# Performance work log

Measured on AMD Instinct MI355X. Metric: run time of the kernel, lower is better.

The kernel has to match this reference:

```python
import jax, jax.numpy as jnp
import numpy as np

K_TOP = 2          # hardcoded k in MyAttentionFunction
S = 32             # hardcoded spatial size (interpolate to 32x32)
N = S * S          # 1024 patches (patch_size=1, stride=1 unfold)
NEG = jnp.float32(-1e30)  # stand-in for excluding columns from top-k


def setup_inputs() -> dict:
    key = jax.random.key(0)
    k1, k2, k3 = jax.random.split(key, 3)
    C = 4096
    generated = jax.random.normal(k1, (1, C, S, S), dtype=jnp.float32)
    known = jax.random.normal(k2, (1, C, S, S), dtype=jnp.float32)
    mask = jax.random.randint(k3, (1, 1, S, S), 0, 2).astype(jnp.float32)
    return {"generated": generated, "known": known, "mask": mask}


def _forward(generated, known, mask):
    C = generated.shape[1]
    # F.interpolate(mask, (32,32)) nearest, then flatten -> flag in {0,1}, shape (N,)
    flag = jax.image.resize(mask, (1, 1, S, S), method="nearest").reshape(N)
    # MyUnfold(x, 1, 1) == [1, N, C]; drop batch dim of 1.
    P = generated.reshape(C, N).T   # (N, C) patches of `generated`
    Kp = known.reshape(C, N).T      # (N, C) patches of `known`

    norm_p = jnp.sum(P * P, axis=-1)   # (N,)
    norm_k = jnp.sum(Kp * Kp, axis=-1)
    # Full cosine matrices; original restricts rows to flag==1 and columns to
    # flag==0 (cosine0) / flag==1 (cosine1) by extraction; we mask columns with
    # a very negative value so top-k returns the same values with GLOBAL indices
    # (which is exactly what the original reconstructs via nonzero()[indexes]).
    cos0 = (P @ Kp.T) / jnp.sqrt(norm_p[:, None] * norm_k[None, :])  # (N, N)
    cos1 = (P @ P.T) / jnp.sqrt(norm_p[:, None] * norm_p[None, :])
    cos0 = jnp.where(flag[None, :] == 0, cos0, NEG)
    cos1 = jnp.where(flag[None, :] == 1, cos1, NEG)

    w0, i0 = jax.lax.top_k(cos0, K_TOP)  # (N, k) values / global indices
    w1, i1 = jax.lax.top_k(cos1, K_TOP)

    m = flag                      # 1.0 on masked rows
    nm = jnp.sum(m)               # number of masked patches
    # weight means taken only over masked rows, then softmax (original uses
    # .item() + numpy softmax, i.e. detached constants).
    means = jnp.stack(
        [jnp.sum(w0[:, i] * m) / nm for i in range(K_TOP)]
        + [jnp.sum(w1[:, i] * m) / nm for i in range(K_TOP)]
    )
    weights = jax.lax.stop_gradient(jax.nn.softmax(means))  # (2k,)

    # The original builds dense 1024x1024 indicator matrices and bmm's them;
    # each indicator row for a masked patch is one-hot at its retrieved source,
    # so the bmm is just a gather into masked rows. The advanced-indexing quirk
    # ind[mask_idx, src_idx] (nonzero() pairs include a leading 0 column) also
    # unconditionally sets ind[0,0]=1; we reproduce that (set semantics: no
    # double count if row 0 already maps to column 0).
    rtn = jnp.zeros((N, C), dtype=generated.dtype)
    for i in range(2 * K_TOP):
        src = Kp if i < K_TOP else P
        cols = (i0 if i < K_TOP else i1)[:, i % K_TOP]  # (N,) global indices
        out_i = jnp.where(m[:, None] == 1, src[cols], 0.0)  # masked rows only
        dup = 1.0 - ((m[0] == 1) & (cols[0] == 0)).astype(src.dtype)
        out_i = out_i.at[0].add(src[0] * dup)  # spurious ind[0,0]=1 artifact
        rtn = rtn + weights[i] * out_i

    rtn = rtn.reshape(1, S, S, C).transpose(0, 3, 1, 2)  # (1, C, 32, 32)
    return jnp.concatenate([generated, known, rtn], axis=1)


def reference(generated, known, mask):
    return _forward(generated, known, mask)
```

## Files before the change

kernel.cpp:

```cpp
#include <hip/hip_runtime.h>
#include <hip/hip_bf16.h>
#include <math.h>

#define N_TOT 1024
#define C_DIM 4096
#define T_MARGIN 3e-4f

typedef __attribute__((ext_vector_type(8))) _Float16 half8;
typedef __attribute__((ext_vector_type(8))) unsigned short ushort8;
typedef __attribute__((ext_vector_type(8))) char schar8;
typedef __attribute__((ext_vector_type(4))) float floatx4;

__device__ inline unsigned short f2h(float v) {
    _Float16 h = (_Float16)v;
    return __builtin_bit_cast(unsigned short, h);
}
__device__ inline float h2f(unsigned short u) {
    return (float)__builtin_bit_cast(_Float16, u);
}
__device__ inline char lo_enc(float v, unsigned short h) {
    int e = (h >> 10) & 31;
    float lo = v - h2f(h);
    float q = rintf(lo * 240.0f * __uint_as_float((unsigned)(152 - e) << 23));
    q = fmaxf(-127.0f, fminf(127.0f, q));
    return (char)(int)q;
}
__device__ inline float lo_dec(char q, unsigned short h) {
    int e = (h >> 10) & 31;
    return (float)q * __uint_as_float((unsigned)(e + 102) << 23) * (1.0f / 240.0f);
}

__global__ __launch_bounds__(256) void flagscan(const float* __restrict__ flag,
                                                int* __restrict__ colidx,
                                                int* __restrict__ n0p) {
    __shared__ int cz[256];
    __shared__ int co[256];
    const int t = threadIdx.x;
    float4 fv = *(const float4*)&flag[4 * t];
    int f[4] = {fv.x == 0.0f, fv.y == 0.0f, fv.z == 0.0f, fv.w == 0.0f};
    int nz = f[0] + f[1] + f[2] + f[3];
    cz[t] = nz; co[t] = 4 - nz;
    __syncthreads();
    for (int off = 1; off < 256; off <<= 1) {
        int vz = (t >= off) ? cz[t - off] : 0;
        int vo = (t >= off) ? co[t - off] : 0;
        __syncthreads();
        cz[t] += vz; co[t] += vo;
        __syncthreads();
    }
    const int n0 = cz[255];
    int zs = cz[t] - nz;
    int os = n0 + co[t] - (4 - nz);
    #pragma unroll
    for (int e = 0; e < 4; e++) {
        int j = 4 * t + e;
        if (f[e]) colidx[zs++] = j;
        else      colidx[os++] = j;
    }
    if (t == 0) *n0p = n0;
}

__global__ __launch_bounds__(256) void split_norms(const float* __restrict__ G,
                                                   const float* __restrict__ Kn,
                                                   unsigned short* __restrict__ Phi,
                                                   char* __restrict__ Plo,
                                                   unsigned short* __restrict__ Khi,
                                                   char* __restrict__ Klo,
                                                   float* __restrict__ normP,
                                                   float* __restrict__ normK) {
    const int z = blockIdx.z;
    const float* X = z ? Kn : G;
    unsigned short* Xhi = z ? Khi : Phi;
    char* Xlo = z ? Klo : Plo;
    float* normX = z ? normK : normP;

    __shared__ float tile[64 * 65];
    __shared__ float np[256];
    const int t  = threadIdx.x;
    const int c0 = blockIdx.x * 64;
    const int n0 = blockIdx.y * 64;

    float s2 = 0.0f;
    #pragma unroll
    for (int s = 0; s < 16; s++) {
        int c_loc = s * 4 + (t >> 6);
        int n_loc = t & 63;
        float v = X[(c0 + c_loc) * N_TOT + n0 + n_loc];
        tile[c_loc * 65 + n_loc] = v;
        s2 = fmaf(v, v, s2);
    }
    np[t] = s2;
    __syncthreads();

    if (t < 64) {
        float tot = np[t] + np[t + 64] + np[t + 128] + np[t + 192];
        atomicAdd(&normX[n0 + t], tot);
    }

    #pragma unroll
    for (int s = 0; s < 4; s++) {
        int n_loc = s * 16 + (t >> 4);
        int c4    = (t & 15) * 4;
        unsigned short h[4]; char l[4];
        #pragma unroll
        for (int e = 0; e < 4; e++) {
            float v = tile[(c4 + e) * 65 + n_loc];
            h[e] = f2h(v);
            l[e] = lo_enc(v, h[e]);
        }
        size_t base = (size_t)(n0 + n_loc) * C_DIM + c0 + c4;
        *(ushort4*)&Xhi[base] = make_ushort4(h[0], h[1], h[2], h[3]);
        *(char4*)&Xlo[base]   = make_char4(l[0], l[1], l[2], l[3]);
    }
}

__global__ __launch_bounds__(256, 4) void gemm_coarse(const unsigned short* __restrict__ Phi,
                                                      const unsigned short* __restrict__ Khi,
                                                      const int* __restrict__ colidx,
                                                      const int* __restrict__ n0p,
                                                      float* __restrict__ dotSel) {
    __shared__ unsigned short sA[64 * 64];
    __shared__ unsigned short sB[128 * 64];

    const int t    = threadIdx.x;
    const int wave = t >> 6, lane = t & 63;
    const int wm   = wave >> 1, wn = wave & 1;
    const int quad = lane >> 4, lrow = lane & 15;
    const int ib = blockIdx.x * 64, jb = blockIdx.y * 128;
    const int k_beg = blockIdx.z * 512;
    const int n0 = *n0p;

    const int srow = t >> 3;
    const int g    = (t & 7) ^ (srow & 7);

    const unsigned short* gA[2];
    gA[0] = Phi + (size_t)(ib + srow) * C_DIM + g * 8;
    gA[1] = gA[0] + (size_t)32 * C_DIM;
    const unsigned short* gB[4];
    #pragma unroll
    for (int q = 0; q < 4; q++) {
        int s = jb + q * 32 + srow;
        int row = colidx[s];
        const unsigned short* src = (s < n0) ? Khi : Phi;
        gB[q] = src + (size_t)row * C_DIM + g * 8;
    }

    floatx4 acc[2][4] = {};

    for (int k0 = k_beg; k0 < k_beg + 512; k0 += 64) {
        #pragma unroll
        for (int q = 0; q < 2; q++)
            __builtin_amdgcn_global_load_lds(
                (const __attribute__((address_space(1))) void*)(gA[q] + k0),
                (__attribute__((address_space(3))) void*)((char*)sA + q * 4096 + t * 16), 16, 0, 0);
        #pragma unroll
        for (int q = 0; q < 4; q++)
            __builtin_amdgcn_global_load_lds(
                (const __attribute__((address_space(1))) void*)(gB[q] + k0),
                (__attribute__((address_space(3))) void*)((char*)sB + q * 4096 + t * 16), 16, 0, 0);
        __syncthreads();

        #pragma unroll
        for (int kk = 0; kk < 2; kk++) {
            const int gk = kk * 4 + quad;
            half8 a[2], b[4];
            #pragma unroll
            for (int ti = 0; ti < 2; ti++) {
                int m = wm * 32 + ti * 16 + lrow;
                a[ti] = *(const half8*)&sA[m * 64 + ((gk ^ (m & 7)) << 3)];
            }
            #pragma unroll
            for (int tj = 0; tj < 4; tj++) {
                int n = wn * 64 + tj * 16 + lrow;
                b[tj] = *(const half8*)&sB[n * 64 + ((gk ^ (n & 7)) << 3)];
            }
            #pragma unroll
            for (int ti = 0; ti < 2; ti++)
                #pragma unroll
                for (int tj = 0; tj < 4; tj++)
                    acc[ti][tj] = __builtin_amdgcn_mfma_f32_16x16x32_f16(a[ti], b[tj], acc[ti][tj], 0, 0, 0);
        }
        __syncthreads();
    }

    #pragma unroll
    for (int tj = 0; tj < 4; tj++) {
        int j = jb + wn * 64 + tj * 16 + lrow;
        #pragma unroll
        for (int ti = 0; ti < 2; ti++) {
            #pragma unroll
            for (int reg = 0; reg < 4; reg++) {
                int i = ib + wm * 32 + ti * 16 + quad * 4 + reg;
                atomicAdd(&dotSel[(size_t)i * N_TOT + j], acc[ti][tj][reg]);
            }
        }
    }
}

__global__ __launch_bounds__(256) void topk_refine(const float* __restrict__ dotSel,
                                                   const unsigned short* __restrict__ Phi,
                                                   const char* __restrict__ Plo,
                                                   const unsigned short* __restrict__ Khi,
                                                   const char* __restrict__ Klo,
                                                   const float* __restrict__ normP,
                                                   const float* __restrict__ normK,
                                                   const int* __restrict__ colidx,
                                                   const int* __restrict__ n0p,
                                                   float* __restrict__ w01,
                                                   int* __restrict__ i01) {
    __shared__ float sAf[C_DIM];
    __shared__ float s_bv[4];
    __shared__ int   s_bj[4];
    __shared__ float s_rcv[8];

    const int row = blockIdx.x;
    const int z   = blockIdx.y;
    const int t   = threadIdx.x;
    const int wave = t >> 6, lane = t & 63;
    const int n0 = *n0p;
    const float nr = normP[row];

    float4 dv = *(const float4*)&dotSel[(size_t)row * N_TOT + 4 * t];
    float cv[4];
    #pragma unroll
    for (int e = 0; e < 4; e++) {
        int s = 4 * t + e;
        bool inz = z ? (s >= n0) : (s < n0);
        if (inz) {
            int gj = colidx[s];
            float nb = (s < n0) ? normK[gj] : normP[gj];
            cv[e] = dv[e] * rsqrtf(nr * nb);
        } else cv[e] = -INFINITY;
    }

    int   cand[8];
    float cval[8];
    #pragma unroll
    for (int it = 0; it < 8; it++) {
        float bv = cv[0]; int bj = 4 * t;
        #pragma unroll
        for (int e = 1; e < 4; e++) {
            int j = 4 * t + e;
            if (cv[e] > bv || (cv[e] == bv && j < bj)) { bv = cv[e]; bj = j; }
        }
        #pragma unroll
        for (int off = 32; off > 0; off >>= 1) {
            float ov = __shfl_xor(bv, off);
            int   oj = __shfl_xor(bj, off);
            if (ov > bv || (ov == bv && oj < bj)) { bv = ov; bj = oj; }
        }
        if (lane == 0) { s_bv[wave] = bv; s_bj[wave] = bj; }
        __syncthreads();
        float wv = s_bv[0]; int wj = s_bj[0];
        #pragma unroll
        for (int w = 1; w < 4; w++)
            if (s_bv[w] > wv || (s_bv[w] == wv && s_bj[w] < wj)) { wv = s_bv[w]; wj = s_bj[w]; }
        cand[it] = wj; cval[it] = wv;
        #pragma unroll
        for (int e = 0; e < 4; e++)
            if (wj == 4 * t + e) cv[e] = -INFINITY;
        __syncthreads();
    }

    const bool trust = (cval[0] - cval[1] > T_MARGIN) && (cval[1] - cval[2] > T_MARGIN);
    if (trust) {
        if (t == 0) {
            int base = (z * N_TOT + row) * 2;
            w01[base]     = cval[0];
            w01[base + 1] = cval[1];
            i01[base]     = colidx[cand[0]];
            i01[base + 1] = colidx[cand[1]];
        }
        return;
    }

    {
        const unsigned short* Ah = Phi + (size_t)row * C_DIM;
        const char*           Al = Plo + (size_t)row * C_DIM;
        #pragma unroll
        for (int s = 0; s < 2; s++) {
            int c = t * 16 + s * 8;
            ushort8 hb = *(const ushort8*)&Ah[c];
            schar8  lb = *(const schar8*)&Al[c];
            #pragma unroll
            for (int e = 0; e < 8; e++) sAf[c + e] = h2f(hb[e]) + lo_dec(lb[e], hb[e]);
        }
    }
    __syncthreads();

    const int grp = t >> 5, l32 = t & 31;
    const int cs  = cand[grp];
    const int gj  = colidx[cs];
    const unsigned short* bh_row = ((cs < n0) ? Khi : Phi) + (size_t)gj * C_DIM;
    const char*           bl_row = ((cs < n0) ? Klo : Plo) + (size_t)gj * C_DIM;
    float acc = 0.0f;
    for (int it = 0; it < 16; it++) {
        int c = it * 256 + l32 * 8;
        ushort8 hb = *(const ushort8*)&bh_row[c];
        schar8  lb = *(const schar8*)&bl_row[c];
        #pragma unroll
        for (int e = 0; e < 8; e++)
            acc = fmaf(sAf[c + e], h2f(hb[e]) + lo_dec(lb[e], hb[e]), acc);
    }
    #pragma unroll
    for (int off = 16; off > 0; off >>= 1) acc += __shfl_xor(acc, off);
    if (l32 == 0) s_rcv[grp] = acc;
    __syncthreads();

    if (t == 0) {
        float v1 = -INFINITY, v2 = -INFINITY;
        int   j1 = 0x7FFFFFFF, j2 = 0x7FFFFFFF;
        #pragma unroll
        for (int q = 0; q < 8; q++) {
            if (!(cval[q] > -1e29f)) continue;
            int s = cand[q];
            int gjx = colidx[s];
            float nb = (s < n0) ? normK[gjx] : normP[gjx];
            float cvx = s_rcv[q] * rsqrtf(nr * nb);
            int j = gjx;
            if (cvx > v1 || (cvx == v1 && j < j1)) {
                v2 = v1; j2 = j1; v1 = cvx; j1 = j;
            } else if (cvx > v2 || (cvx == v2 && j < j2)) {
                v2 = cvx; j2 = j;
            }
        }
        int base = (z * N_TOT + row) * 2;
        w01[base]     = v1;
        w01[base + 1] = v2;
        i01[base]     = j1;
        i01[base + 1] = j2;
    }
}

__global__ __launch_bounds__(256) void output_kernel(const float* __restrict__ G,
                                                     const float* __restrict__ Kn,
                                                     const float* __restrict__ flag,
                                                     const float* __restrict__ w01,
                                                     const int* __restrict__ i01,
                                                     float* __restrict__ out) {
    __shared__ float red[5][4];
    __shared__ float wts[4];
    const int c  = blockIdx.x;
    const int t  = threadIdx.x;
    const int n4 = t * 4;

    float4 fv = *(const float4*)&flag[n4];
    const float fa[4] = {fv.x, fv.y, fv.z, fv.w};

    float pm[5] = {};
    #pragma unroll
    for (int e = 0; e < 4; e++) {
        int n = n4 + e;
        float m = fa[e];
        pm[0] += m;
        pm[1] += m * w01[n * 2 + 0];
        pm[2] += m * w01[n * 2 + 1];
        pm[3] += m * w01[2 * N_TOT + n * 2 + 0];
        pm[4] += m * w01[2 * N_TOT + n * 2 + 1];
    }
    #pragma unroll
    for (int i = 0; i < 5; i++)
        #pragma unroll
        for (int off = 32; off > 0; off >>= 1)
            pm[i] += __shfl_xor(pm[i], off);
    const int wave = t >> 6, lane = t & 63;
    if (lane == 0) {
        #pragma unroll
        for (int i = 0; i < 5; i++) red[i][wave] = pm[i];
    }
    __syncthreads();
    if (t == 0) {
        float tot[5];
        #pragma unroll
        for (int i = 0; i < 5; i++)
            tot[i] = red[i][0] + red[i][1] + red[i][2] + red[i][3];
        float inv = 1.0f / tot[0];
        float mv[4] = {tot[1] * inv, tot[2] * inv, tot[3] * inv, tot[4] * inv};
        float mx = fmaxf(fmaxf(mv[0], mv[1]), fmaxf(mv[2], mv[3]));
        float e[4], s = 0.0f;
        #pragma unroll
        for (int q = 0; q < 4; q++) { e[q] = expf(mv[q] - mx); s += e[q]; }
        #pragma unroll
        for (int q = 0; q < 4; q++) wts[q] = e[q] / s;
    }
    __syncthreads();
    const float w0 = wts[0], w1 = wts[1], w2 = wts[2], w3 = wts[3];

    float4 gv = *(const float4*)&G[c * N_TOT + n4];
    float4 kv = *(const float4*)&Kn[c * N_TOT + n4];
    *(float4*)&out[c * N_TOT + n4] = gv;
    *(float4*)&out[C_DIM * N_TOT + c * N_TOT + n4] = kv;

    float val[4];
    #pragma unroll
    for (int e = 0; e < 4; e++) {
        int n = n4 + e;
        float v = 0.0f;
        if (fa[e] == 1.0f) {
            int c00 = i01[n * 2 + 0];
            int c01 = i01[n * 2 + 1];
            int c10 = i01[2 * N_TOT + n * 2 + 0];
            int c11 = i01[2 * N_TOT + n * 2 + 1];
            v = w0 * Kn[c * N_TOT + c00] + w1 * Kn[c * N_TOT + c01]
              + w2 * G[c * N_TOT + c10]  + w3 * G[c * N_TOT + c11];
        }
        if (n == 0) {
            bool m0 = (flag[0] == 1.0f);
            int c00 = i01[0], c01 = i01[1];
            int c10 = i01[2 * N_TOT], c11 = i01[2 * N_TOT + 1];
            float kn0 = Kn[c * N_TOT];
            float g0  = G[c * N_TOT];
            if (!(m0 && c00 == 0)) v += w0 * kn0;
            if (!(m0 && c01 == 0)) v += w1 * kn0;
            if (!(m0 && c10 == 0)) v += w2 * g0;
            if (!(m0 && c11 == 0)) v += w3 * g0;
        }
        val[e] = v;
    }
    *(float4*)&out[2 * C_DIM * N_TOT + c * N_TOT + n4] =
        make_float4(val[0], val[1], val[2], val[3]);
}

extern "C" void kernel_launch(void* const* d_in, const int* in_sizes, int n_in,
                              void* d_out, int out_size, void* d_ws, size_t ws_size,
                              hipStream_t stream) {
    const float* G    = (const float*)d_in[0];
    const float* Kn   = (const float*)d_in[1];
    const float* flag = (const float*)d_in[2];
    float* out = (float*)d_out;

    char* p = (char*)d_ws;
    unsigned short* Phi = (unsigned short*)p;  p += (size_t)N_TOT * C_DIM * 2;
    unsigned short* Khi = (unsigned short*)p;  p += (size_t)N_TOT * C_DIM * 2;
    char* Plo = p;                             p += (size_t)N_TOT * C_DIM;
    char* Klo = p;                             p += (size_t)N_TOT * C_DIM;
    float* dotSel = (float*)p;                 p += (size_t)N_TOT * N_TOT * 4;
    float* normP  = (float*)p;                 p += N_TOT * 4;
    float* normK  = (float*)p;                 p += N_TOT * 4;
    float* w01    = (float*)p;                 p += 4 * N_TOT * 4;
    int*   i01    = (int*)p;                   p += 4 * N_TOT * 4;
    int*   colidx = (int*)p;                   p += N_TOT * 4;
    int*   n0p    = (int*)p;

    const size_t zero_bytes = ((size_t)N_TOT * N_TOT + 2 * N_TOT) * sizeof(float);
    hipMemsetAsync(dotSel, 0, zero_bytes, stream);

    flagscan<<<1, 256, 0, stream>>>(flag, colidx, n0p);
    split_norms<<<dim3(64, 16, 2), 256, 0, stream>>>(G, Kn, Phi, Plo, Khi, Klo, normP, normK);
    gemm_coarse<<<dim3(16, 8, 8), 256, 0, stream>>>(Phi, Khi, colidx, n0p, dotSel);
    topk_refine<<<dim3(1024, 2), 256, 0, stream>>>(dotSel, Phi, Plo, Khi, Klo,
                                                   normP, normK, colidx, n0p, w01, i01);
    output_kernel<<<4096, 256, 0, stream>>>(G, Kn, flag, w01, i01, out);
}
```

Measured before the change: 186.0 us.

## Replace split-K atomics with partial buffers, fuse flagscan, merge top-k passes

The GEMM's split-K slices now write plain stores into eight separate partial buffers instead of atomically adding into one zeroed matrix. The top-k kernel sums those partials once per row and handles both column groups in a single block. This removes the 4MB memset, the atomic traffic and the duplicate dot-row reads. The flag scan is folded into the first block of split_norms to save a launch, at the cost of 32MB of extra partial-buffer writes and reads.

```diff
diff --git a/kernel.cpp b/kernel.cpp
--- a/kernel.cpp
+++ b/kernel.cpp
@@ -30,44 +30,17 @@
     return (float)q * __uint_as_float((unsigned)(e + 102) << 23) * (1.0f / 240.0f);
 }
 
-__global__ __launch_bounds__(256) void flagscan(const float* __restrict__ flag,
-                                                int* __restrict__ colidx,
-                                                int* __restrict__ n0p) {
-    __shared__ int cz[256];
-    __shared__ int co[256];
-    const int t = threadIdx.x;
-    float4 fv = *(const float4*)&flag[4 * t];
-    int f[4] = {fv.x == 0.0f, fv.y == 0.0f, fv.z == 0.0f, fv.w == 0.0f};
-    int nz = f[0] + f[1] + f[2] + f[3];
-    cz[t] = nz; co[t] = 4 - nz;
-    __syncthreads();
-    for (int off = 1; off < 256; off <<= 1) {
-        int vz = (t >= off) ? cz[t - off] : 0;
-        int vo = (t >= off) ? co[t - off] : 0;
-        __syncthreads();
-        cz[t] += vz; co[t] += vo;
-        __syncthreads();
-    }
-    const int n0 = cz[255];
-    int zs = cz[t] - nz;
-    int os = n0 + co[t] - (4 - nz);
-    #pragma unroll
-    for (int e = 0; e < 4; e++) {
-        int j = 4 * t + e;
-        if (f[e]) colidx[zs++] = j;
-        else      colidx[os++] = j;
-    }
-    if (t == 0) *n0p = n0;
-}
-
 __global__ __launch_bounds__(256) void split_norms(const float* __restrict__ G,
                                                    const float* __restrict__ Kn,
+                                                   const float* __restrict__ flag,
                                                    unsigned short* __restrict__ Phi,
                                                    char* __restrict__ Plo,
                                                    unsigned short* __restrict__ Khi,
                                                    char* __restrict__ Klo,
                                                    float* __restrict__ normP,
-                                                   float* __restrict__ normK) {
+                                                   float* __restrict__ normK,
+                                                   int* __restrict__ colidx,
+                                                   int* __restrict__ n0p) {
     const int z = blockIdx.z;
     const float* X = z ? Kn : G;
     unsigned short* Xhi = z ? Khi : Phi;
@@ -112,13 +85,40 @@
         *(ushort4*)&Xhi[base] = make_ushort4(h[0], h[1], h[2], h[3]);
         *(char4*)&Xlo[base]   = make_char4(l[0], l[1], l[2], l[3]);
     }
+
+    if (blockIdx.x == 0 && blockIdx.y == 0 && blockIdx.z == 0) {
+        __shared__ int cz[256];
+        __shared__ int co[256];
+        float4 fv = *(const float4*)&flag[4 * t];
+        int f[4] = {fv.x == 0.0f, fv.y == 0.0f, fv.z == 0.0f, fv.w == 0.0f};
+        int nz = f[0] + f[1] + f[2] + f[3];
+        cz[t] = nz; co[t] = 4 - nz;
+        __syncthreads();
+        for (int off = 1; off < 256; off <<= 1) {
+            int vz = (t >= off) ? cz[t - off] : 0;
+            int vo = (t >= off) ? co[t - off] : 0;
+            __syncthreads();
+            cz[t] += vz; co[t] += vo;
+            __syncthreads();
+        }
+        const int fn0 = cz[255];
+        int zs = cz[t] - nz;
+        int os = fn0 + co[t] - (4 - nz);
+        #pragma unroll
+        for (int e = 0; e < 4; e++) {
+            int j = 4 * t + e;
+            if (f[e]) colidx[zs++] = j;
+            else      colidx[os++] = j;
+        }
+        if (t == 0) *n0p = fn0;
+    }
 }
 
 __global__ __launch_bounds__(256, 4) void gemm_coarse(const unsigned short* __restrict__ Phi,
                                                       const unsigned short* __restrict__ Khi,
                                                       const int* __restrict__ colidx,
                                                       const int* __restrict__ n0p,
-                                                      float* __restrict__ dotSel) {
+                                                      float* __restrict__ dotPart) {
     __shared__ unsigned short sA[64 * 64];
     __shared__ unsigned short sB[128 * 64];
 
@@ -127,7 +127,8 @@
     const int wm   = wave >> 1, wn = wave & 1;
     const int quad = lane >> 4, lrow = lane & 15;
     const int ib = blockIdx.x * 64, jb = blockIdx.y * 128;
-    const int k_beg = blockIdx.z * 512;
+    const int bz = blockIdx.z;
+    const int k_beg = bz * 512;
     const int n0 = *n0p;
 
     const int srow = t >> 3;
@@ -183,6 +184,7 @@
         __syncthreads();
     }
 
+    float* outp = dotPart + ((size_t)bz << 20);
     #pragma unroll
     for (int tj = 0; tj < 4; tj++) {
         int j = jb + wn * 64 + tj * 16 + lrow;
@@ -191,13 +193,13 @@
             #pragma unroll
             for (int reg = 0; reg < 4; reg++) {
                 int i = ib + wm * 32 + ti * 16 + quad * 4 + reg;
-                atomicAdd(&dotSel[(size_t)i * N_TOT + j], acc[ti][tj][reg]);
-            }
-        }
-    }
-}
-
-__global__ __launch_bounds__(256) void topk_refine(const float* __restrict__ dotSel,
+                outp[i * N_TOT + j] = acc[ti][tj][reg];
+            }
+        }
+    }
+}
+
+__global__ __launch_bounds__(256) void topk_refine(const float* __restrict__ dotPart,
                                                    const unsigned short* __restrict__ Phi,
                                                    const char* __restrict__ Plo,
                                                    const unsigned short* __restrict__ Khi,
@@ -214,65 +216,80 @@
     __shared__ float s_rcv[8];
 
     const int row = blockIdx.x;
-    const int z   = blockIdx.y;
     const int t   = threadIdx.x;
     const int wave = t >> 6, lane = t & 63;
     const int n0 = *n0p;
     const float nr = normP[row];
 
-    float4 dv = *(const float4*)&dotSel[(size_t)row * N_TOT + 4 * t];
+    float4 dv = make_float4(0.f, 0.f, 0.f, 0.f);
+    #pragma unroll
+    for (int z = 0; z < 8; z++) {
+        float4 p = *(const float4*)&dotPart[((size_t)z << 20) + (size_t)row * N_TOT + 4 * t];
+        dv.x += p.x; dv.y += p.y; dv.z += p.z; dv.w += p.w;
+    }
+
     float cv[4];
     #pragma unroll
     for (int e = 0; e < 4; e++) {
         int s = 4 * t + e;
-        bool inz = z ? (s >= n0) : (s < n0);
-        if (inz) {
-            int gj = colidx[s];
-            float nb = (s < n0) ? normK[gj] : normP[gj];
-            cv[e] = dv[e] * rsqrtf(nr * nb);
-        } else cv[e] = -INFINITY;
-    }
-
-    int   cand[8];
-    float cval[8];
-    #pragma unroll
-    for (int it = 0; it < 8; it++) {
-        float bv = cv[0]; int bj = 4 * t;
-        #pragma unroll
-        for (int e = 1; e < 4; e++) {
-            int j = 4 * t + e;
-            if (cv[e] > bv || (cv[e] == bv && j < bj)) { bv = cv[e]; bj = j; }
-        }
-        #pragma unroll
-        for (int off = 32; off > 0; off >>= 1) {
-            float ov = __shfl_xor(bv, off);
-            int   oj = __shfl_xor(bj, off);
-            if (ov > bv || (ov == bv && oj < bj)) { bv = ov; bj = oj; }
-        }
-        if (lane == 0) { s_bv[wave] = bv; s_bj[wave] = bj; }
-        __syncthreads();
-        float wv = s_bv[0]; int wj = s_bj[0];
-        #pragma unroll
-        for (int w = 1; w < 4; w++)
-            if (s_bv[w] > wv || (s_bv[w] == wv && s_bj[w] < wj)) { wv = s_bv[w]; wj = s_bj[w]; }
-        cand[it] = wj; cval[it] = wv;
-        #pragma unroll
-        for (int e = 0; e < 4; e++)
-            if (wj == 4 * t + e) cv[e] = -INFINITY;
-        __syncthreads();
-    }
-
-    const bool trust = (cval[0] - cval[1] > T_MARGIN) && (cval[1] - cval[2] > T_MARGIN);
-    if (trust) {
-        if (t == 0) {
-            int base = (z * N_TOT + row) * 2;
-            w01[base]     = cval[0];
-            w01[base + 1] = cval[1];
-            i01[base]     = colidx[cand[0]];
-            i01[base + 1] = colidx[cand[1]];
-        }
-        return;
-    }
+        int gj = colidx[s];
+        float nb = (s < n0) ? normK[gj] : normP[gj];
+        float d  = (e == 0) ? dv.x : (e == 1) ? dv.y : (e == 2) ? dv.z : dv.w;
+        cv[e] = d * rsqrtf(nr * nb);
+    }
+
+    int   candZ[2][8];
+    float cvalZ[2][8];
+    bool  need[2];
+
+    #pragma unroll
+    for (int zz = 0; zz < 2; zz++) {
+        float mv[4];
+        #pragma unroll
+        for (int e = 0; e < 4; e++) {
+            int s = 4 * t + e;
+            bool inz = zz ? (s >= n0) : (s < n0);
+            mv[e] = inz ? cv[e] : -INFINITY;
+        }
+        #pragma unroll
+        for (int it = 0; it < 8; it++) {
+            float bv = mv[0]; int bj = 4 * t;
+            #pragma unroll
+            for (int e = 1; e < 4; e++) {
+                int j = 4 * t + e;
+                if (mv[e] > bv || (mv[e] == bv && j < bj)) { bv = mv[e]; bj = j; }
+            }
+            #pragma unroll
+            for (int off = 32; off > 0; off >>= 1) {
+                float ov = __shfl_xor(bv, off);
+                int   oj = __shfl_xor(bj, off);
+                if (ov > bv || (ov == bv && oj < bj)) { bv = ov; bj = oj; }
+            }
+            if (lane == 0) { s_bv[wave] = bv; s_bj[wave] = bj; }
+            __syncthreads();
+            float wv = s_bv[0]; int wj = s_bj[0];
+            #pragma unroll
+            for (int w = 1; w < 4; w++)
+                if (s_bv[w] > wv || (s_bv[w] == wv && s_bj[w] < wj)) { wv = s_bv[w]; wj = s_bj[w]; }
+            candZ[zz][it] = wj; cvalZ[zz][it] = wv;
+            #pragma unroll
+            for (int e = 0; e < 4; e++)
+                if (wj == 4 * t + e) mv[e] = -INFINITY;
+            __syncthreads();
+        }
+        const bool trust = (cvalZ[zz][0] - cvalZ[zz][1] > T_MARGIN) &&
+                           (cvalZ[zz][1] - cvalZ[zz][2] > T_MARGIN);
+        need[zz] = !trust;
+        if (trust && t == 0) {
+            int base = (zz * N_TOT + row) * 2;
+            w01[base]     = cvalZ[zz][0];
+            w01[base + 1] = cvalZ[zz][1];
+            i01[base]     = colidx[candZ[zz][0]];
+            i01[base + 1] = colidx[candZ[zz][1]];
+        }
+    }
+
+    if (!need[0] && !need[1]) return;
 
     {
         const unsigned short* Ah = Phi + (size_t)row * C_DIM;
@@ -288,47 +305,52 @@
     }
     __syncthreads();
 
-    const int grp = t >> 5, l32 = t & 31;
-    const int cs  = cand[grp];
-    const int gj  = colidx[cs];
-    const unsigned short* bh_row = ((cs < n0) ? Khi : Phi) + (size_t)gj * C_DIM;
-    const char*           bl_row = ((cs < n0) ? Klo : Plo) + (size_t)gj * C_DIM;
-    float acc = 0.0f;
-    for (int it = 0; it < 16; it++) {
-        int c = it * 256 + l32 * 8;
-        ushort8 hb = *(const ushort8*)&bh_row[c];
-        schar8  lb = *(const schar8*)&bl_row[c];
-        #pragma unroll
-        for (int e = 0; e < 8; e++)
-            acc = fmaf(sAf[c + e], h2f(hb[e]) + lo_dec(lb[e], hb[e]), acc);
-    }
-    #pragma unroll
-    for (int off = 16; off > 0; off >>= 1) acc += __shfl_xor(acc, off);
-    if (l32 == 0) s_rcv[grp] = acc;
-    __syncthreads();
-
-    if (t == 0) {
-        float v1 = -INFINITY, v2 = -INFINITY;
-        int   j1 = 0x7FFFFFFF, j2 = 0x7FFFFFFF;
-        #pragma unroll
-        for (int q = 0; q < 8; q++) {
-            if (!(cval[q] > -1e29f)) continue;
-            int s = cand[q];
-            int gjx = colidx[s];
-            float nb = (s < n0) ? normK[gjx] : normP[gjx];
-            float cvx = s_rcv[q] * rsqrtf(nr * nb);
-            int j = gjx;
-            if (cvx > v1 || (cvx == v1 && j < j1)) {
-                v2 = v1; j2 = j1; v1 = cvx; j1 = j;
-            } else if (cvx > v2 || (cvx == v2 && j < j2)) {
-                v2 = cvx; j2 = j;
-            }
-        }
-        int base = (z * N_TOT + row) * 2;
-        w01[base]     = v1;
-        w01[base + 1] = v2;
-        i01[base]     = j1;
-        i01[base + 1] = j2;
+    #pragma unroll
+    for (int zz = 0; zz < 2; zz++) {
+        if (!need[zz]) continue;
+        const int grp = t >> 5, l32 = t & 31;
+        const int cs  = candZ[zz][grp];
+        const int gj  = colidx[cs];
+        const unsigned short* bh_row = ((cs < n0) ? Khi : Phi) + (size_t)gj * C_DIM;
+        const char*           bl_row = ((cs < n0) ? Klo : Plo) + (size_t)gj * C_DIM;
+        float acc = 0.0f;
+        for (int it = 0; it < 16; it++) {
+            int c = it * 256 + l32 * 8;
+            ushort8 hb = *(const ushort8*)&bh_row[c];
+            schar8  lb = *(const schar8*)&bl_row[c];
+            #pragma unroll
+            for (int e = 0; e < 8; e++)
+                acc = fmaf(sAf[c + e], h2f(hb[e]) + lo_dec(lb[e], hb[e]), acc);
+        }
+        #pragma unroll
+        for (int off = 16; off > 0; off >>= 1) acc += __shfl_xor(acc, off);
+        if (l32 == 0) s_rcv[grp] = acc;
+        __syncthreads();
+
+        if (t == 0) {
+            float v1 = -INFINITY, v2 = -INFINITY;
+            int   j1 = 0x7FFFFFFF, j2 = 0x7FFFFFFF;
+            #pragma unroll
+            for (int q = 0; q < 8; q++) {
+                if (!(cvalZ[zz][q] > -1e29f)) continue;
+                int s = candZ[zz][q];
+                int gjx = colidx[s];
+                float nb = (s < n0) ? normK[gjx] : normP[gjx];
+                float cvx = s_rcv[q] * rsqrtf(nr * nb);
+                int j = gjx;
+                if (cvx > v1 || (cvx == v1 && j < j1)) {
+                    v2 = v1; j2 = j1; v1 = cvx; j1 = j;
+                } else if (cvx > v2 || (cvx == v2 && j < j2)) {
+                    v2 = cvx; j2 = j;
+                }
+            }
+            int base = (zz * N_TOT + row) * 2;
+            w01[base]     = v1;
+            w01[base + 1] = v2;
+            i01[base]     = j1;
+            i01[base + 1] = j2;
+        }
+        __syncthreads();
     }
 }
 
@@ -434,7 +456,7 @@
     unsigned short* Khi = (unsigned short*)p;  p += (size_t)N_TOT * C_DIM * 2;
     char* Plo = p;                             p += (size_t)N_TOT * C_DIM;
     char* Klo = p;                             p += (size_t)N_TOT * C_DIM;
-    float* dotSel = (float*)p;                 p += (size_t)N_TOT * N_TOT * 4;
+    float* dotPart = (float*)p;                p += (size_t)8 * N_TOT * N_TOT * 4;
     float* normP  = (float*)p;                 p += N_TOT * 4;
     float* normK  = (float*)p;                 p += N_TOT * 4;
     float* w01    = (float*)p;                 p += 4 * N_TOT * 4;
@@ -442,13 +464,12 @@
     int*   colidx = (int*)p;                   p += N_TOT * 4;
     int*   n0p    = (int*)p;
 
-    const size_t zero_bytes = ((size_t)N_TOT * N_TOT + 2 * N_TOT) * sizeof(float);
-    hipMemsetAsync(dotSel, 0, zero_bytes, stream);
-
-    flagscan<<<1, 256, 0, stream>>>(flag, colidx, n0p);
-    split_norms<<<dim3(64, 16, 2), 256, 0, stream>>>(G, Kn, Phi, Plo, Khi, Klo, normP, normK);
-    gemm_coarse<<<dim3(16, 8, 8), 256, 0, stream>>>(Phi, Khi, colidx, n0p, dotSel);
-    topk_refine<<<dim3(1024, 2), 256, 0, stream>>>(dotSel, Phi, Plo, Khi, Klo,
-                                                   normP, normK, colidx, n0p, w01, i01);
+    hipMemsetAsync(normP, 0, 2 * N_TOT * sizeof(float), stream);
+
+    split_norms<<<dim3(64, 16, 2), 256, 0, stream>>>(G, Kn, flag, Phi, Plo, Khi, Klo,
+                                                     normP, normK, colidx, n0p);
+    gemm_coarse<<<dim3(16, 8, 8), 256, 0, stream>>>(Phi, Khi, colidx, n0p, dotPart);
+    topk_refine<<<1024, 256, 0, stream>>>(dotPart, Phi, Plo, Khi, Klo,
+                                          normP, normK, colidx, n0p, w01, i01);
     output_kernel<<<4096, 256, 0, stream>>>(G, Kn, flag, w01, i01, out);
 }
```

New measurement: 176.0 us. 1.06x faster.
